# Kernel tuning notes

Measured on AMD Instinct MI355X. Metric: run time of the kernel, lower is better.

## Reference

```python
import jax, jax.numpy as jnp
import numpy as np

NA, NKPT, NC = 3, 17, 1
NO_DET = NC + 5              # 6
NO = NO_DET + 3 * NKPT       # 57
ANCHORS = np.array([[19,27,44,40,38,94],[96,68,86,152,180,137],[140,301,303,264,238,542]], dtype=np.float32).reshape(3, 3, 2)
STRIDES = np.array([8.0, 16.0, 32.0], dtype=np.float32)
CH = (256, 512, 1024)
HW = (80, 40, 20)
B = 16


def setup_inputs():
    key = jax.random.key(0)
    ks = jax.random.split(key, 18)
    d = {}
    ki = 0
    for i, (c, hw) in enumerate(zip(CH, HW)):
        d[f"f{i}"] = jax.random.normal(ks[ki], (B, c, hw, hw), jnp.float32); ki += 1
        d[f"ia{i}"] = jax.random.normal(ks[ki], (1, c, 1, 1), jnp.float32) * 0.02; ki += 1
        d[f"w{i}"] = jax.random.normal(ks[ki], (NA * NO_DET, c), jnp.float32) * (1.0 / np.sqrt(c)); ki += 1
        d[f"b{i}"] = jnp.zeros((NA * NO_DET,), jnp.float32)
        d[f"im{i}"] = 1.0 + jax.random.normal(ks[ki], (1, NA * NO_DET, 1, 1), jnp.float32) * 0.02; ki += 1
        d[f"wk{i}"] = jax.random.normal(ks[ki], (NA * 3 * NKPT, c), jnp.float32) * (1.0 / np.sqrt(c)); ki += 1
        d[f"bk{i}"] = jnp.zeros((NA * 3 * NKPT,), jnp.float32)
    return d


def _decode(feat, ia, w, b, im, wk, bk, anchors_l, stride):
    # ImplicitA -> 1x1 conv -> ImplicitM (det branch); plain 1x1 conv (kpt branch)
    det = jnp.einsum('bchw,oc->bohw', feat + ia, w) + b[None, :, None, None]
    det = det * im
    kpt = jnp.einsum('bchw,oc->bohw', feat, wk) + bk[None, :, None, None]
    x = jnp.concatenate([det, kpt], axis=1)          # (B, na*no, H, W)
    Bb, _, H, W = x.shape
    x = x.reshape(Bb, NA, NO, H, W).transpose(0, 1, 3, 4, 2)  # (B, na, H, W, no)
    yv, xv = jnp.meshgrid(jnp.arange(H), jnp.arange(W), indexing='ij')
    grid = jnp.stack([xv, yv], -1).astype(x.dtype)[None, None]  # (1,1,H,W,2)
    xd = jax.nn.sigmoid(x[..., :NO_DET])
    xy = (xd[..., 0:2] * 2.0 - 0.5 + grid) * stride
    wh = (xd[..., 2:4] * 2.0) ** 2 * anchors_l.reshape(1, NA, 1, 1, 2)
    kp = x[..., NO_DET:]                              # (B, na, H, W, 51)
    kx = (kp[..., 0::3] * 2.0 - 0.5 + grid[..., 0:1]) * stride
    ky = (kp[..., 1::3] * 2.0 - 0.5 + grid[..., 1:2]) * stride
    kc = jax.nn.sigmoid(kp[..., 2::3])
    kdec = jnp.stack([kx, ky, kc], -1).reshape(Bb, NA, H, W, 3 * NKPT)
    y = jnp.concatenate([xy, wh, xd[..., 4:], kdec], -1)  # (B, na, H, W, 57)
    return y.reshape(Bb, -1, NO)


def reference(f0, ia0, w0, b0, im0, wk0, bk0,
              f1, ia1, w1, b1, im1, wk1, bk1,
              f2, ia2, w2, b2, im2, wk2, bk2):
    anchors = jnp.asarray(ANCHORS)
    z0 = _decode(f0, ia0, w0, b0, im0, wk0, bk0, anchors[0], STRIDES[0])
    z1 = _decode(f1, ia1, w1, b1, im1, wk1, bk1, anchors[1], STRIDES[1])
    z2 = _decode(f2, ia2, w2, b2, im2, wk2, bk2, anchors[2], STRIDES[2])
    return jnp.concatenate([z0, z1, z2], axis=1)      # (B, 25200, 57)
```

## Files before the change

kernel.cpp:

```cpp
#include <hip/hip_runtime.h>
#include <hip/hip_bf16.h>

typedef __attribute__((ext_vector_type(8))) short short8;
typedef __attribute__((ext_vector_type(4))) float floatx4;

__device__ __forceinline__ float sigm(float x) { return 1.0f / (1.0f + __expf(-x)); }

__device__ __forceinline__ unsigned short f2bf(float v) {
  union { __hip_bfloat16 h; unsigned short u; } cv;
  cv.h = __float2bfloat16(v);
  return cv.u;
}

__device__ __forceinline__ void glds16(const void* g, void* l) {
  __builtin_amdgcn_global_load_lds((const __attribute__((address_space(1))) void*)g,
                                   (__attribute__((address_space(3))) void*)l, 16, 0, 0);
}

struct PrepArgs {
  const float *w, *b, *im, *ia, *wk, *bk;
  unsigned short* Wp;
  float* bias;
  int C;
};

__global__ void prep_kernel(PrepArgs A0, PrepArgs A1, PrepArgs A2) {
  PrepArgs A = (blockIdx.y == 0) ? A0 : (blockIdx.y == 1) ? A1 : A2;
  const int n = blockIdx.x;
  const int t = threadIdx.x;
  const int C = A.C;
  unsigned short* wrow = A.Wp + (size_t)n * C;
  if (n >= 171) {
    for (int k = t; k < C; k += 64) wrow[k] = 0;
    if (t == 0) A.bias[n] = 0.0f;
    return;
  }
  if (n < 18) {
    const float* src = A.w + (size_t)n * C;
    const float sc = A.im[n];
    float dot = 0.0f;
    for (int k = t; k < C; k += 64) {
      float v = src[k];
      dot += v * A.ia[k];
      wrow[k] = f2bf(v * sc);
    }
#pragma unroll
    for (int off = 32; off > 0; off >>= 1) dot += __shfl_down(dot, off);
    if (t == 0) A.bias[n] = sc * (A.b[n] + dot);
  } else {
    const float* src = A.wk + (size_t)(n - 18) * C;
    for (int k = t; k < C; k += 64) wrow[k] = f2bf(src[k]);
    if (t == 0) A.bias[n] = A.bk[n - 18];
  }
}

#define LDS_BYTES 49152

template <int SC, int C, int HW, int W>
__device__ __forceinline__ void gemm_decode(const float* __restrict__ feat,
                                            const unsigned short* __restrict__ Wp,
                                            const float* __restrict__ bias,
                                            float* __restrict__ out, int tile, char* smem) {
  constexpr float STRD = (SC == 0) ? 8.0f : (SC == 1) ? 16.0f : 32.0f;
  constexpr int ZOFF = (SC == 0) ? 0 : (SC == 1) ? 19200 : 24000;
  constexpr int I = C / 64;

  const int t = threadIdx.x;
  const int lane = t & 63;
  const int wv = t >> 6;
  const int l15 = lane & 15;
  const int quad = lane >> 4;

  char* BB = smem;
  float* Elds = (float*)smem;

  const int mA = tile * 64 + wv * 16 + l15;
  const int bA = mA / HW;
  const int pA = mA - bA * HW;
  const float* fbase = feat + ((size_t)bA * C + quad * 8) * (size_t)HW + pA;

  const int rsub = lane >> 3;
  const int csw = (lane & 7) ^ rsub;
  const char* WpB = (const char*)Wp;

  floatx4 acc[11];
#pragma unroll
  for (int nj = 0; nj < 11; ++nj) acc[nj] = (floatx4){0.f, 0.f, 0.f, 0.f};

  const int c0 = quad ^ (l15 & 7);
  const int bOff0 = l15 * 128 + c0 * 16;
  const int bOff1 = l15 * 128 + (c0 ^ 4) * 16;

  float v[16];
  auto loadA = [&](int it) {
    const float* g = fbase + (size_t)it * 64 * HW;
#pragma unroll
    for (int j = 0; j < 8; ++j) {
      v[j] = g[(size_t)j * HW];
      v[j + 8] = g[(size_t)(32 + j) * HW];
    }
  };
  auto stageB = [&](int it, int buf) {
#pragma unroll
    for (int j = 0; j < 6; ++j) {
      const int rowb = wv * 48 + j * 8;
      const void* gsrc = WpB + ((size_t)(rowb + rsub) * C + (size_t)it * 64) * 2 + csw * 16;
      glds16(gsrc, BB + buf * 24576 + rowb * 128);
    }
  };

  stageB(0, 0);
  loadA(0);

  for (int it = 0; it < I; ++it) {
    asm volatile("s_waitcnt vmcnt(16)\n\ts_barrier" ::: "memory");
    stageB((it + 1 < I) ? it + 1 : 0, (it + 1) & 1);
    __builtin_amdgcn_sched_barrier(0);
    short8 af0, af1;
#pragma unroll
    for (int j = 0; j < 8; ++j) {
      af0[j] = (short)f2bf(v[j]);
      af1[j] = (short)f2bf(v[j + 8]);
    }
    __builtin_amdgcn_sched_barrier(0);
    loadA((it + 1 < I) ? it + 1 : it);
    __builtin_amdgcn_sched_barrier(0);
    const char* bBase = BB + (it & 1) * 24576;
#pragma unroll
    for (int nj = 0; nj < 11; ++nj) {
      short8 b0 = *(const short8*)(bBase + bOff0 + (size_t)nj * 2048);
      short8 b1 = *(const short8*)(bBase + bOff1 + (size_t)nj * 2048);
      acc[nj] = __builtin_amdgcn_mfma_f32_16x16x32_bf16(af0, b0, acc[nj], 0, 0, 0);
      acc[nj] = __builtin_amdgcn_mfma_f32_16x16x32_bf16(af1, b1, acc[nj], 0, 0, 0);
    }
  }

  float bj[11];
#pragma unroll
  for (int nj = 0; nj < 11; ++nj) bj[nj] = bias[nj * 16 + l15];

#pragma unroll
  for (int c = 0; c < 2; ++c) {
    __syncthreads();
    if ((wv >> 1) == c) {
      const int rbase = (wv & 1) * 16 + quad * 4;
#pragma unroll
      for (int nj = 0; nj < 11; ++nj)
#pragma unroll
        for (int r = 0; r < 4; ++r)
          Elds[(rbase + r) * 180 + nj * 16 + l15] = acc[nj][r] + bj[nj];
    }
    __syncthreads();
    if (t < 192) {
      const int task = t >> 1, half = t & 1;
      const int row = task & 31, a = task >> 5;
      const int m = tile * 64 + c * 32 + row;
      const int bb = m / HW;
      const int p = m - bb * HW;
      const float fx = (float)(p % W);
      const float fy = (float)(p / W);
      float* L = Elds + row * 180 + a * 57;
      if (half == 0) {
        float aw, ah;
        if constexpr (SC == 0) {
          aw = (a == 0) ? 19.f : (a == 1) ? 44.f : 38.f;
          ah = (a == 0) ? 27.f : (a == 1) ? 40.f : 94.f;
        } else if constexpr (SC == 1) {
          aw = (a == 0) ? 96.f : (a == 1) ? 86.f : 180.f;
          ah = (a == 0) ? 68.f : (a == 1) ? 152.f : 137.f;
        } else {
          aw = (a == 0) ? 140.f : (a == 1) ? 303.f : 238.f;
          ah = (a == 0) ? 301.f : (a == 1) ? 264.f : 542.f;
        }
        float r0 = L[0], r1 = L[1], r2 = L[2], r3 = L[3], r4 = L[4], r5 = L[5];
        L[0] = (sigm(r0) * 2.f - 0.5f + fx) * STRD;
        L[1] = (sigm(r1) * 2.f - 0.5f + fy) * STRD;
        float tw = sigm(r2) * 2.f;
        L[2] = tw * tw * aw;
        float th = sigm(r3) * 2.f;
        L[3] = th * th * ah;
        L[4] = sigm(r4);
        L[5] = sigm(r5);
#pragma unroll
        for (int kp = 0; kp < 8; ++kp) {
          float kx = L[6 + 3 * kp], ky = L[7 + 3 * kp], kc = L[8 + 3 * kp];
          L[6 + 3 * kp] = (kx * 2.f - 0.5f + fx) * STRD;
          L[7 + 3 * kp] = (ky * 2.f - 0.5f + fy) * STRD;
          L[8 + 3 * kp] = sigm(kc);
        }
      } else {
#pragma unroll
        for (int kp = 8; kp < 17; ++kp) {
          float kx = L[6 + 3 * kp], ky = L[7 + 3 * kp], kc = L[8 + 3 * kp];
          L[6 + 3 * kp] = (kx * 2.f - 0.5f + fx) * STRD;
          L[7 + 3 * kp] = (ky * 2.f - 0.5f + fy) * STRD;
          L[8 + 3 * kp] = sigm(kc);
        }
      }
    }
    __syncthreads();
    for (int i = t; i < 96 * 57; i += 256) {
      int sr = i / 57;
      int j = i - sr * 57;
      int a = sr >> 5, row = sr & 31;
      int m = tile * 64 + c * 32 + row;
      int bb = m / HW;
      int p = m - bb * HW;
      out[((size_t)bb * 25200 + (size_t)(ZOFF + a * HW + p)) * 57 + j] =
          Elds[row * 180 + a * 57 + j];
    }
  }
}

__global__ __launch_bounds__(256, 3) void main_kernel(
    const float* __restrict__ f0, const float* __restrict__ f1, const float* __restrict__ f2,
    const unsigned short* __restrict__ Wp0, const unsigned short* __restrict__ Wp1,
    const unsigned short* __restrict__ Wp2, const float* __restrict__ b0,
    const float* __restrict__ b1, const float* __restrict__ b2, float* __restrict__ out) {
  __shared__ __align__(16) char smem[LDS_BYTES];
  const int bid = blockIdx.x;
  if (bid < 100)
    gemm_decode<2, 1024, 400, 20>(f2, Wp2, b2, out, bid, smem);
  else if (bid < 500)
    gemm_decode<1, 512, 1600, 40>(f1, Wp1, b1, out, bid - 100, smem);
  else
    gemm_decode<0, 256, 6400, 80>(f0, Wp0, b0, out, bid - 500, smem);
}

extern "C" void kernel_launch(void* const* d_in, const int* in_sizes, int n_in, void* d_out,
                              int out_size, void* d_ws, size_t ws_size, hipStream_t stream) {
  const float *f[3], *ia[3], *w[3], *b[3], *im[3], *wk[3], *bk[3];
  for (int s = 0; s < 3; ++s) {
    f[s] = (const float*)d_in[7 * s + 0];
    ia[s] = (const float*)d_in[7 * s + 1];
    w[s] = (const float*)d_in[7 * s + 2];
    b[s] = (const float*)d_in[7 * s + 3];
    im[s] = (const float*)d_in[7 * s + 4];
    wk[s] = (const float*)d_in[7 * s + 5];
    bk[s] = (const float*)d_in[7 * s + 6];
  }
  char* ws = (char*)d_ws;
  unsigned short* Wp0 = (unsigned short*)(ws + 0);
  unsigned short* Wp1 = (unsigned short*)(ws + 98304);
  unsigned short* Wp2 = (unsigned short*)(ws + 294912);
  float* bias0 = (float*)(ws + 688128);
  float* bias1 = (float*)(ws + 688896);
  float* bias2 = (float*)(ws + 689664);

  PrepArgs A0 = {w[0], b[0], im[0], ia[0], wk[0], bk[0], Wp0, bias0, 256};
  PrepArgs A1 = {w[1], b[1], im[1], ia[1], wk[1], bk[1], Wp1, bias1, 512};
  PrepArgs A2 = {w[2], b[2], im[2], ia[2], wk[2], bk[2], Wp2, bias2, 1024};
  prep_kernel<<<dim3(192, 3), 64, 0, stream>>>(A0, A1, A2);

  main_kernel<<<2100, 256, 0, stream>>>(f[0], f[1], f[2], Wp0, Wp1, Wp2, bias0, bias1, bias2,
                                        (float*)d_out);
}
```

Before: 296.9 us.

## Pre-swizzle weights into MFMA fragment layout and read B directly from global

```diff
diff --git a/kernel.cpp b/kernel.cpp
--- a/kernel.cpp
+++ b/kernel.cpp
@@ -12,9 +12,11 @@
   return cv.u;
 }
 
-__device__ __forceinline__ void glds16(const void* g, void* l) {
-  __builtin_amdgcn_global_load_lds((const __attribute__((address_space(1))) void*)g,
-                                   (__attribute__((address_space(3))) void*)l, 16, 0, 0);
+__device__ __forceinline__ size_t boff(int n, int k) {
+  const int nj = n >> 4, l15 = n & 15;
+  const int it = k >> 6, kk = k & 63;
+  const int h = kk >> 5, quad = (kk >> 3) & 3, j = kk & 7;
+  return ((size_t)((it * 11 + nj) * 2 + h) * 512) + (size_t)(quad * 16 + l15) * 8 + j;
 }
 
 struct PrepArgs {
@@ -29,9 +31,8 @@
   const int n = blockIdx.x;
   const int t = threadIdx.x;
   const int C = A.C;
-  unsigned short* wrow = A.Wp + (size_t)n * C;
   if (n >= 171) {
-    for (int k = t; k < C; k += 64) wrow[k] = 0;
+    for (int k = t; k < C; k += 64) A.Wp[boff(n, k)] = 0;
     if (t == 0) A.bias[n] = 0.0f;
     return;
   }
@@ -42,19 +43,19 @@
     for (int k = t; k < C; k += 64) {
       float v = src[k];
       dot += v * A.ia[k];
-      wrow[k] = f2bf(v * sc);
+      A.Wp[boff(n, k)] = f2bf(v * sc);
     }
 #pragma unroll
     for (int off = 32; off > 0; off >>= 1) dot += __shfl_down(dot, off);
     if (t == 0) A.bias[n] = sc * (A.b[n] + dot);
   } else {
     const float* src = A.wk + (size_t)(n - 18) * C;
-    for (int k = t; k < C; k += 64) wrow[k] = f2bf(src[k]);
+    for (int k = t; k < C; k += 64) A.Wp[boff(n, k)] = f2bf(src[k]);
     if (t == 0) A.bias[n] = A.bk[n - 18];
   }
 }
 
-#define LDS_BYTES 49152
+#define LDS_BYTES 23040
 
 template <int SC, int C, int HW, int W>
 __device__ __forceinline__ void gemm_decode(const float* __restrict__ feat,
@@ -71,7 +72,6 @@
   const int l15 = lane & 15;
   const int quad = lane >> 4;
 
-  char* BB = smem;
   float* Elds = (float*)smem;
 
   const int mA = tile * 64 + wv * 16 + l15;
@@ -79,17 +79,11 @@
   const int pA = mA - bA * HW;
   const float* fbase = feat + ((size_t)bA * C + quad * 8) * (size_t)HW + pA;
 
-  const int rsub = lane >> 3;
-  const int csw = (lane & 7) ^ rsub;
-  const char* WpB = (const char*)Wp;
+  const char* Bbase = (const char*)Wp + lane * 16;
 
   floatx4 acc[11];
 #pragma unroll
   for (int nj = 0; nj < 11; ++nj) acc[nj] = (floatx4){0.f, 0.f, 0.f, 0.f};
-
-  const int c0 = quad ^ (l15 & 7);
-  const int bOff0 = l15 * 128 + c0 * 16;
-  const int bOff1 = l15 * 128 + (c0 ^ 4) * 16;
 
   float v[16];
   auto loadA = [&](int it) {
@@ -100,36 +94,23 @@
       v[j + 8] = g[(size_t)(32 + j) * HW];
     }
   };
-  auto stageB = [&](int it, int buf) {
-#pragma unroll
-    for (int j = 0; j < 6; ++j) {
-      const int rowb = wv * 48 + j * 8;
-      const void* gsrc = WpB + ((size_t)(rowb + rsub) * C + (size_t)it * 64) * 2 + csw * 16;
-      glds16(gsrc, BB + buf * 24576 + rowb * 128);
-    }
-  };
-
-  stageB(0, 0);
+
   loadA(0);
-
+#pragma unroll 1
   for (int it = 0; it < I; ++it) {
-    asm volatile("s_waitcnt vmcnt(16)\n\ts_barrier" ::: "memory");
-    stageB((it + 1 < I) ? it + 1 : 0, (it + 1) & 1);
-    __builtin_amdgcn_sched_barrier(0);
     short8 af0, af1;
 #pragma unroll
     for (int j = 0; j < 8; ++j) {
       af0[j] = (short)f2bf(v[j]);
       af1[j] = (short)f2bf(v[j + 8]);
     }
+    if (it + 1 < I) loadA(it + 1);
     __builtin_amdgcn_sched_barrier(0);
-    loadA((it + 1 < I) ? it + 1 : it);
-    __builtin_amdgcn_sched_barrier(0);
-    const char* bBase = BB + (it & 1) * 24576;
+    const char* bp = Bbase + (size_t)it * 22528;
 #pragma unroll
     for (int nj = 0; nj < 11; ++nj) {
-      short8 b0 = *(const short8*)(bBase + bOff0 + (size_t)nj * 2048);
-      short8 b1 = *(const short8*)(bBase + bOff1 + (size_t)nj * 2048);
+      short8 b0 = *(const short8*)(bp + nj * 2048);
+      short8 b1 = *(const short8*)(bp + nj * 2048 + 1024);
       acc[nj] = __builtin_amdgcn_mfma_f32_16x16x32_bf16(af0, b0, acc[nj], 0, 0, 0);
       acc[nj] = __builtin_amdgcn_mfma_f32_16x16x32_bf16(af1, b1, acc[nj], 0, 0, 0);
     }
@@ -212,7 +193,7 @@
   }
 }
 
-__global__ __launch_bounds__(256, 3) void main_kernel(
+__global__ __launch_bounds__(256, 4) void main_kernel(
     const float* __restrict__ f0, const float* __restrict__ f1, const float* __restrict__ f2,
     const unsigned short* __restrict__ Wp0, const unsigned short* __restrict__ Wp1,
     const unsigned short* __restrict__ Wp2, const float* __restrict__ b0,
@@ -250,7 +231,7 @@
   PrepArgs A0 = {w[0], b[0], im[0], ia[0], wk[0], bk[0], Wp0, bias0, 256};
   PrepArgs A1 = {w[1], b[1], im[1], ia[1], wk[1], bk[1], Wp1, bias1, 512};
   PrepArgs A2 = {w[2], b[2], im[2], ia[2], wk[2], bk[2], Wp2, bias2, 1024};
-  prep_kernel<<<dim3(192, 3), 64, 0, stream>>>(A0, A1, A2);
+  prep_kernel<<<dim3(176, 3), 64, 0, stream>>>(A0, A1, A2);
 
   main_kernel<<<2100, 256, 0, stream>>>(f[0], f[1], f[2], Wp0, Wp1, Wp2, bias0, bias1, bias2,
                                         (float*)d_out);
```

New measurement: 316.0 us. 1.06x slower.

## Shrink K-step and LDS footprint to raise occupancy in fused conv-decode kernel

Applied to the files above, without the earlier changes.

```diff
diff --git a/kernel.cpp b/kernel.cpp
--- a/kernel.cpp
+++ b/kernel.cpp
@@ -54,7 +54,7 @@
   }
 }
 
-#define LDS_BYTES 49152
+#define LDS_BYTES 11520
 
 template <int SC, int C, int HW, int W>
 __device__ __forceinline__ void gemm_decode(const float* __restrict__ feat,
@@ -63,7 +63,7 @@
                                             float* __restrict__ out, int tile, char* smem) {
   constexpr float STRD = (SC == 0) ? 8.0f : (SC == 1) ? 16.0f : 32.0f;
   constexpr int ZOFF = (SC == 0) ? 0 : (SC == 1) ? 19200 : 24000;
-  constexpr int I = C / 64;
+  constexpr int I = C / 32;
 
   const int t = threadIdx.x;
   const int lane = t & 63;
@@ -79,59 +79,53 @@
   const int pA = mA - bA * HW;
   const float* fbase = feat + ((size_t)bA * C + quad * 8) * (size_t)HW + pA;
 
-  const int rsub = lane >> 3;
-  const int csw = (lane & 7) ^ rsub;
+  const int rsub = lane >> 2;
+  const int csw = (lane & 3) ^ (rsub & 3);
   const char* WpB = (const char*)Wp;
+  const int g0 = wv * 3;
+  const int ng = (wv == 3) ? 2 : 3;
 
   floatx4 acc[11];
 #pragma unroll
   for (int nj = 0; nj < 11; ++nj) acc[nj] = (floatx4){0.f, 0.f, 0.f, 0.f};
 
-  const int c0 = quad ^ (l15 & 7);
-  const int bOff0 = l15 * 128 + c0 * 16;
-  const int bOff1 = l15 * 128 + (c0 ^ 4) * 16;
-
-  float v[16];
+  const char* bRd = BB + l15 * 64 + (quad ^ (l15 & 3)) * 16;
+
+  float v[8];
   auto loadA = [&](int it) {
-    const float* g = fbase + (size_t)it * 64 * HW;
-#pragma unroll
-    for (int j = 0; j < 8; ++j) {
-      v[j] = g[(size_t)j * HW];
-      v[j + 8] = g[(size_t)(32 + j) * HW];
-    }
+    const float* g = fbase + (size_t)it * 32 * HW;
+#pragma unroll
+    for (int j = 0; j < 8; ++j) v[j] = g[(size_t)j * HW];
   };
-  auto stageB = [&](int it, int buf) {
-#pragma unroll
-    for (int j = 0; j < 6; ++j) {
-      const int rowb = wv * 48 + j * 8;
-      const void* gsrc = WpB + ((size_t)(rowb + rsub) * C + (size_t)it * 64) * 2 + csw * 16;
-      glds16(gsrc, BB + buf * 24576 + rowb * 128);
+  auto stageB = [&](int it) {
+#pragma unroll
+    for (int g = 0; g < 3; ++g) {
+      if (g < ng) {
+        const int grp = g0 + g;
+        const void* gsrc =
+            WpB + ((size_t)(grp * 16 + rsub) * C + (size_t)it * 32) * 2 + csw * 16;
+        glds16(gsrc, BB + grp * 1024);
+      }
     }
   };
 
-  stageB(0, 0);
   loadA(0);
-
+#pragma unroll 1
   for (int it = 0; it < I; ++it) {
-    asm volatile("s_waitcnt vmcnt(16)\n\ts_barrier" ::: "memory");
-    stageB((it + 1 < I) ? it + 1 : 0, (it + 1) & 1);
+    asm volatile("s_barrier" ::: "memory");
+    stageB(it);
     __builtin_amdgcn_sched_barrier(0);
-    short8 af0, af1;
-#pragma unroll
-    for (int j = 0; j < 8; ++j) {
-      af0[j] = (short)f2bf(v[j]);
-      af1[j] = (short)f2bf(v[j + 8]);
-    }
+    short8 af;
+#pragma unroll
+    for (int j = 0; j < 8; ++j) af[j] = (short)f2bf(v[j]);
     __builtin_amdgcn_sched_barrier(0);
     loadA((it + 1 < I) ? it + 1 : it);
     __builtin_amdgcn_sched_barrier(0);
-    const char* bBase = BB + (it & 1) * 24576;
+    asm volatile("s_waitcnt vmcnt(8)\n\ts_barrier" ::: "memory");
 #pragma unroll
     for (int nj = 0; nj < 11; ++nj) {
-      short8 b0 = *(const short8*)(bBase + bOff0 + (size_t)nj * 2048);
-      short8 b1 = *(const short8*)(bBase + bOff1 + (size_t)nj * 2048);
-      acc[nj] = __builtin_amdgcn_mfma_f32_16x16x32_bf16(af0, b0, acc[nj], 0, 0, 0);
-      acc[nj] = __builtin_amdgcn_mfma_f32_16x16x32_bf16(af1, b1, acc[nj], 0, 0, 0);
+      short8 b = *(const short8*)(bRd + nj * 1024);
+      acc[nj] = __builtin_amdgcn_mfma_f32_16x16x32_bf16(af, b, acc[nj], 0, 0, 0);
     }
   }
 
@@ -139,28 +133,26 @@
 #pragma unroll
   for (int nj = 0; nj < 11; ++nj) bj[nj] = bias[nj * 16 + l15];
 
-#pragma unroll
-  for (int c = 0; c < 2; ++c) {
+  for (int c = 0; c < 4; ++c) {
     __syncthreads();
-    if ((wv >> 1) == c) {
-      const int rbase = (wv & 1) * 16 + quad * 4;
+    if (wv == c) {
 #pragma unroll
       for (int nj = 0; nj < 11; ++nj)
 #pragma unroll
         for (int r = 0; r < 4; ++r)
-          Elds[(rbase + r) * 180 + nj * 16 + l15] = acc[nj][r] + bj[nj];
+          Elds[(quad * 4 + r) * 180 + nj * 16 + l15] = acc[nj][r] + bj[nj];
     }
     __syncthreads();
     if (t < 192) {
-      const int task = t >> 1, half = t & 1;
-      const int row = task & 31, a = task >> 5;
-      const int m = tile * 64 + c * 32 + row;
+      const int task = t >> 2, sub = t & 3;
+      const int row = task & 15, a = task >> 4;
+      const int m = tile * 64 + c * 16 + row;
       const int bb = m / HW;
       const int p = m - bb * HW;
       const float fx = (float)(p % W);
       const float fy = (float)(p / W);
       float* L = Elds + row * 180 + a * 57;
-      if (half == 0) {
+      if (sub == 0) {
         float aw, ah;
         if constexpr (SC == 0) {
           aw = (a == 0) ? 19.f : (a == 1) ? 44.f : 38.f;
@@ -181,16 +173,10 @@
         L[3] = th * th * ah;
         L[4] = sigm(r4);
         L[5] = sigm(r5);
-#pragma unroll
-        for (int kp = 0; kp < 8; ++kp) {
-          float kx = L[6 + 3 * kp], ky = L[7 + 3 * kp], kc = L[8 + 3 * kp];
-          L[6 + 3 * kp] = (kx * 2.f - 0.5f + fx) * STRD;
-          L[7 + 3 * kp] = (ky * 2.f - 0.5f + fy) * STRD;
-          L[8 + 3 * kp] = sigm(kc);
-        }
       } else {
-#pragma unroll
-        for (int kp = 8; kp < 17; ++kp) {
+        const int kb = (sub - 1) * 6;
+        const int ke = (sub == 3) ? 17 : kb + 6;
+        for (int kp = kb; kp < ke; ++kp) {
           float kx = L[6 + 3 * kp], ky = L[7 + 3 * kp], kc = L[8 + 3 * kp];
           L[6 + 3 * kp] = (kx * 2.f - 0.5f + fx) * STRD;
           L[7 + 3 * kp] = (ky * 2.f - 0.5f + fy) * STRD;
@@ -199,11 +185,11 @@
       }
     }
     __syncthreads();
-    for (int i = t; i < 96 * 57; i += 256) {
+    for (int i = t; i < 48 * 57; i += 256) {
       int sr = i / 57;
       int j = i - sr * 57;
-      int a = sr >> 5, row = sr & 31;
-      int m = tile * 64 + c * 32 + row;
+      int a = sr >> 4, row = sr & 15;
+      int m = tile * 64 + c * 16 + row;
       int bb = m / HW;
       int p = m - bb * HW;
       out[((size_t)bb * 25200 + (size_t)(ZOFF + a * HW + p)) * 57 + j] =
@@ -212,7 +198,7 @@
   }
 }
 
-__global__ __launch_bounds__(256, 3) void main_kernel(
+__global__ __launch_bounds__(256, 8) void main_kernel(
     const float* __restrict__ f0, const float* __restrict__ f1, const float* __restrict__ f2,
     const unsigned short* __restrict__ Wp0, const unsigned short* __restrict__ Wp1,
     const unsigned short* __restrict__ Wp2, const float* __restrict__ b0,
@@ -250,7 +236,7 @@
   PrepArgs A0 = {w[0], b[0], im[0], ia[0], wk[0], bk[0], Wp0, bias0, 256};
   PrepArgs A1 = {w[1], b[1], im[1], ia[1], wk[1], bk[1], Wp1, bias1, 512};
   PrepArgs A2 = {w[2], b[2], im[2], ia[2], wk[2], bk[2], Wp2, bias2, 1024};
-  prep_kernel<<<dim3(192, 3), 64, 0, stream>>>(A0, A1, A2);
+  prep_kernel<<<dim3(176, 3), 64, 0, stream>>>(A0, A1, A2);
 
   main_kernel<<<2100, 256, 0, stream>>>(f[0], f[1], f[2], Wp0, Wp1, Wp2, bias0, bias1, bias2,
                                         (float*)d_out);
```

New measurement: 352.6 us. +18.8%, slower.
